# Performance work log

Hardware: AMD Instinct MI355X
Metric: run time of the kernel (lower is better)

The kernel has to match this reference:

```python
import jax, jax.numpy as jnp
import numpy as np

N = 50000      # nodes
E = 800000     # edges
H, C = 4, 32   # heads, per-head channels
NF = 513       # n_fft//2 + 1 frequency bins
NMEL = 128
NEG_SLOPE_ATT = 0.2   # GATConv leaky_relu slope
NEG_SLOPE_MLP = 0.01  # F.leaky_relu default


def setup_inputs() -> dict:
    key = jax.random.key(0)
    ks = jax.random.split(key, 12)
    s = 0.05
    return {
        "x": jax.random.normal(ks[0], (N, NF), jnp.float32),
        "edge_index": jax.random.randint(ks[1], (2, E), 0, N, dtype=jnp.int32),
        "fb": jax.random.normal(ks[2], (NF, NMEL), jnp.float32) * s,
        "Wg": jax.random.normal(ks[3], (NMEL, H * C), jnp.float32) * s,
        "bias_g": jnp.zeros((H * C,), jnp.float32),
        "att_src": jax.random.normal(ks[4], (H, C), jnp.float32) * s,
        "att_dst": jax.random.normal(ks[5], (H, C), jnp.float32) * s,
        "W1": jax.random.normal(ks[6], (H * C, 256), jnp.float32) * s,
        "b1": jnp.zeros((256,), jnp.float32),
        "W2": jax.random.normal(ks[7], (256, 128), jnp.float32) * s,
        "b2": jnp.zeros((128,), jnp.float32),
        "W3": jax.random.normal(ks[8], (128, 10), jnp.float32) * s,
        "b3": jnp.zeros((10,), jnp.float32),
    }


def gat_conv(h, src, dst, att_src, att_dst, bias_g):
    # h: [N, H, C]; per-edge attention, segment softmax over dst, scatter-add
    a_s = jnp.einsum('nhc,hc->nh', h, att_src)  # [N, H]
    a_d = jnp.einsum('nhc,hc->nh', h, att_dst)  # [N, H]
    e = jax.nn.leaky_relu(a_s[src] + a_d[dst], NEG_SLOPE_ATT)  # [E', H]
    m = jax.ops.segment_max(e, dst, num_segments=N)            # [N, H]
    ex = jnp.exp(e - m[dst])
    denom = jax.ops.segment_sum(ex, dst, num_segments=N)       # [N, H]
    alpha = ex / denom[dst]                                    # [E', H]
    msg = h[src] * alpha[:, :, None]                           # [E', H, C]
    out = jax.ops.segment_sum(msg, dst, num_segments=N)        # [N, H, C]
    return out.reshape(N, H * C) + bias_g


def reference(x, edge_index, fb, Wg, bias_g, att_src, att_dst, W1, b1, W2, b2, W3, b3):
    # learnable mel filterbank projection: [N, NF] -> [N, NMEL]
    x = x @ fb
    # GATConv linear transform, split into heads
    h = (x @ Wg).reshape(N, H, C)
    # add self loops (PyG GATConv default add_self_loops=True)
    loop = jnp.arange(N, dtype=edge_index.dtype)
    src = jnp.concatenate([edge_index[0], loop])
    dst = jnp.concatenate([edge_index[1], loop])
    x = jax.nn.elu(gat_conv(h, src, dst, att_src, att_dst, bias_g))
    # dropout is identity in eval mode
    x = jax.nn.leaky_relu(x @ W1 + b1, NEG_SLOPE_MLP)
    x = jax.nn.leaky_relu(x @ W2 + b2, NEG_SLOPE_MLP)
    x = jax.nn.leaky_relu(x @ W3 + b3, NEG_SLOPE_MLP)
    return jax.nn.softmax(x, axis=-1)
```

## Files before the change

### kernel.cpp

```cpp
#include <hip/hip_runtime.h>
#include <hip/hip_bf16.h>

#define NN 50000
#define EE 800000
#define NFR 513
#define NMEL 128
#define HC 128

typedef __bf16 bf16x8 __attribute__((ext_vector_type(8)));
typedef float floatx4 __attribute__((ext_vector_type(4)));

__device__ __forceinline__ unsigned short f2b(float f) {
    unsigned u = __float_as_uint(f);
    u = (u + 0x7FFFu + ((u >> 16) & 1u)) >> 16;
    return (unsigned short)u;
}
__device__ __forceinline__ float b2f(unsigned short s) {
    return __uint_as_float(((unsigned)s) << 16);
}
__device__ __forceinline__ float lexp(float a) {
    a = a > 0.f ? a : 0.2f * a;
    return __expf(a);
}

__device__ __forceinline__ float ldf(const float* p, long i) { return p[i]; }
__device__ __forceinline__ void stf(float* p, long i, float v) { p[i] = v; }
__device__ __forceinline__ void stf(__hip_bfloat16* p, long i, float v) {
    ((unsigned short*)p)[i] = f2b(v);
}

#define BM 64
#define BN 64
#define BK 16

template<int EPI, typename TA, typename TB, typename TC>
__global__ __launch_bounds__(256) void gemm_k(const TA* __restrict__ A, const TB* __restrict__ B,
                                              TC* __restrict__ C, int M, int Nn, int K,
                                              const float* __restrict__ bias)
{
    __shared__ float As[BK][BM + 4];
    __shared__ float Bs[BK][BN + 4];
    const int t = threadIdx.x;
    const int row0 = blockIdx.x * BM;
    const int col0 = blockIdx.y * BN;
    const int tc = t & 15, tr = t >> 4;
    float acc[4][4] = {};

    for (int kb = 0; kb < K; kb += BK) {
        #pragma unroll
        for (int i = 0; i < 4; ++i) {
            int idx = i * 256 + t;
            int r = idx >> 4, k = idx & 15;
            int gr = row0 + r, gk = kb + k;
            float v = 0.f;
            if (gr < M && gk < K) v = ldf(A, (long)gr * K + gk);
            As[k][r] = v;
        }
        #pragma unroll
        for (int i = 0; i < 4; ++i) {
            int idx = i * 256 + t;
            int c = idx & 63, k = idx >> 6;
            int gk = kb + k, gc = col0 + c;
            float v = 0.f;
            if (gk < K && gc < Nn) v = ldf(B, (long)gk * Nn + gc);
            Bs[k][c] = v;
        }
        __syncthreads();
        #pragma unroll
        for (int kk = 0; kk < BK; ++kk) {
            float4 av = *reinterpret_cast<const float4*>(&As[kk][tr << 2]);
            float4 bv = *reinterpret_cast<const float4*>(&Bs[kk][tc << 2]);
            float a[4] = {av.x, av.y, av.z, av.w};
            float b[4] = {bv.x, bv.y, bv.z, bv.w};
            #pragma unroll
            for (int i = 0; i < 4; ++i)
                #pragma unroll
                for (int j = 0; j < 4; ++j)
                    acc[i][j] += a[i] * b[j];
        }
        __syncthreads();
    }

    #pragma unroll
    for (int i = 0; i < 4; ++i) {
        int gr = row0 + (tr << 2) + i;
        if (gr >= M) continue;
        #pragma unroll
        for (int j = 0; j < 4; ++j) {
            int gc = col0 + (tc << 2) + j;
            if (gc >= Nn) continue;
            float v = acc[i][j];
            if (EPI == 2) {
                stf(C, (long)gc * 544 + gr, v);
            } else {
                if (EPI == 1) { v += bias[gc]; v = v > 0.f ? v : 0.01f * v; }
                stf(C, (long)gr * Nn + gc, v);
            }
        }
    }
}

__global__ void k_trans(const float* __restrict__ in, __hip_bfloat16* __restrict__ outp,
                        int K, int N, int KP)
{
    int id = blockIdx.x * 256 + threadIdx.x;
    if (id >= N * KP) return;
    int n = id / KP, k = id % KP;
    float v = (k < K) ? in[(long)k * N + n] : 0.f;
    ((unsigned short*)outp)[id] = f2b(v);
}

#define PS 40

__device__ __forceinline__ void stageA_t(const float* A, unsigned short* As, int t,
                                         int row0, int M, int K, int kb)
{
    #pragma unroll
    for (int g = 0; g < 2; ++g) {
        int q = g * 256 + t;
        int row = q >> 3, k4 = (q & 7) * 4;
        int gr = row0 + row, gk = kb + k4;
        ushort4 pk = make_ushort4(0, 0, 0, 0);
        if (gr < M) {
            const float* ap = A + (long)gr * K + gk;
            if (gk + 3 < K) {
                pk.x = f2b(ap[0]); pk.y = f2b(ap[1]); pk.z = f2b(ap[2]); pk.w = f2b(ap[3]);
            } else {
                if (gk + 0 < K) pk.x = f2b(ap[0]);
                if (gk + 1 < K) pk.y = f2b(ap[1]);
                if (gk + 2 < K) pk.z = f2b(ap[2]);
            }
        }
        *reinterpret_cast<ushort4*>(&As[row * PS + k4]) = pk;
    }
}

__device__ __forceinline__ void stageA_t(const __hip_bfloat16* A, unsigned short* As, int t,
                                         int row0, int M, int K, int kb)
{
    int c = t;
    int row = c >> 2, k8 = (c & 3) * 8;
    int gr = row0 + row;
    uint4 val = make_uint4(0, 0, 0, 0);
    if (gr < M) val = *reinterpret_cast<const uint4*>(A + (long)gr * K + kb + k8);
    *reinterpret_cast<uint4*>(&As[row * PS + k8]) = val;
}

template<int EPI, typename TA, typename TC>
__global__ __launch_bounds__(256) void mgemm(const TA* __restrict__ A,
                                             const __hip_bfloat16* __restrict__ Bt,
                                             TC* __restrict__ C,
                                             int M, int Nn, int K, int KB,
                                             const float* __restrict__ bias)
{
    __shared__ unsigned short As[64 * PS];
    __shared__ unsigned short Bs[128 * PS];
    const int t = threadIdx.x;
    const int row0 = blockIdx.x * 64;
    const int col0 = blockIdx.y * 128;
    const int wave = t >> 6, lane = t & 63;
    const int wm = (wave >> 1) * 32, wn = (wave & 1) * 64;
    const int lm = lane & 15, kq = lane >> 4;

    floatx4 acc[2][4];
    #pragma unroll
    for (int i = 0; i < 2; ++i)
        #pragma unroll
        for (int j = 0; j < 4; ++j)
            acc[i][j] = 0.f;

    for (int kb = 0; kb < KB; kb += 32) {
        stageA_t(A, As, t, row0, M, K, kb);
        #pragma unroll
        for (int g = 0; g < 2; ++g) {
            int c = g * 256 + t;
            int row = c >> 2, k8 = (c & 3) * 8;
            int gn = col0 + row;
            uint4 val = make_uint4(0, 0, 0, 0);
            if (gn < Nn) val = *reinterpret_cast<const uint4*>(Bt + (long)gn * KB + kb + k8);
            *reinterpret_cast<uint4*>(&Bs[row * PS + k8]) = val;
        }
        __syncthreads();

        bf16x8 af[2], bf[4];
        #pragma unroll
        for (int i = 0; i < 2; ++i)
            af[i] = *reinterpret_cast<const bf16x8*>(&As[(wm + i * 16 + lm) * PS + kq * 8]);
        #pragma unroll
        for (int j = 0; j < 4; ++j)
            bf[j] = *reinterpret_cast<const bf16x8*>(&Bs[(wn + j * 16 + lm) * PS + kq * 8]);
        #pragma unroll
        for (int i = 0; i < 2; ++i)
            #pragma unroll
            for (int j = 0; j < 4; ++j)
                acc[i][j] = __builtin_amdgcn_mfma_f32_16x16x32_bf16(af[i], bf[j], acc[i][j], 0, 0, 0);
        __syncthreads();
    }

    #pragma unroll
    for (int i = 0; i < 2; ++i) {
        #pragma unroll
        for (int r = 0; r < 4; ++r) {
            int gr = row0 + wm + i * 16 + kq * 4 + r;
            if (gr >= M) continue;
            #pragma unroll
            for (int j = 0; j < 4; ++j) {
                int gc = col0 + wn + j * 16 + lm;
                float v = acc[i][j][r];
                if (EPI == 1) { v += bias[gc]; v = v > 0.f ? v : 0.01f * v; }
                stf(C, (long)gr * Nn + gc, v);
            }
        }
    }
}

__global__ void k_att(const __hip_bfloat16* __restrict__ h, const float* __restrict__ att_src,
                      const float* __restrict__ att_dst,
                      float* __restrict__ a_s, float* __restrict__ a_d)
{
    int id = blockIdx.x * blockDim.x + threadIdx.x;
    if (id >= NN * 4) return;
    int n = id >> 2, hh = id & 3;
    const unsigned short* hr = (const unsigned short*)(h + (long)n * HC + hh * 32);
    float s1 = 0.f, s2 = 0.f;
    #pragma unroll
    for (int c = 0; c < 32; ++c) {
        float v = b2f(hr[c]);
        s1 += v * att_src[hh * 32 + c];
        s2 += v * att_dst[hh * 32 + c];
    }
    a_s[id] = s1;
    a_d[id] = s2;
}

__global__ void k_hist(const int* __restrict__ ei, int* __restrict__ hist)
{
    int e = blockIdx.x * 256 + threadIdx.x;
    if (e < EE) atomicAdd(&hist[ei[EE + e]], 1);
}

__global__ __launch_bounds__(512) void k_scan1(const int* __restrict__ hist, int* __restrict__ start,
                                               int* __restrict__ aux)
{
    __shared__ int sm[512];
    int t = threadIdx.x, i = blockIdx.x * 512 + t;
    int v = (i < NN) ? hist[i] : 0;
    sm[t] = v;
    __syncthreads();
    for (int off = 1; off < 512; off <<= 1) {
        int x = (t >= off) ? sm[t - off] : 0;
        __syncthreads();
        sm[t] += x;
        __syncthreads();
    }
    if (i < NN) start[i] = sm[t] - v;
    if (t == 511) aux[blockIdx.x] = sm[511];
}

__global__ void k_scan2(int* __restrict__ aux, int nb)
{
    if (blockIdx.x == 0 && threadIdx.x == 0) {
        int run = 0;
        for (int b = 0; b < nb; ++b) { int v = aux[b]; aux[b] = run; run += v; }
    }
}

__global__ __launch_bounds__(512) void k_scan3(int* __restrict__ start, int* __restrict__ cursor,
                                               const int* __restrict__ aux)
{
    int i = blockIdx.x * 512 + threadIdx.x;
    if (i < NN) {
        int v = start[i] + aux[blockIdx.x];
        start[i] = v;
        cursor[i] = v;
    }
    if (i == 0) start[NN] = EE;
}

__global__ void k_fill(const int* __restrict__ ei, int* __restrict__ cursor, int* __restrict__ sorted)
{
    int e = blockIdx.x * 256 + threadIdx.x;
    if (e >= EE) return;
    int s = ei[e], d = ei[EE + e];
    int pos = atomicAdd(&cursor[d], 1);
    sorted[pos] = s;
}

__global__ __launch_bounds__(256) void k_agg(const int* __restrict__ start, const int* __restrict__ sorted,
                                             const float* __restrict__ a_s, const float* __restrict__ a_d,
                                             const __hip_bfloat16* __restrict__ h,
                                             const float* __restrict__ bias_g,
                                             __hip_bfloat16* __restrict__ agg)
{
    int wave = threadIdx.x >> 6;
    int lane = threadIdx.x & 63;
    int d = blockIdx.x * 4 + wave;
    if (d >= NN) return;
    int hh = lane >> 4;
    float ad = a_d[d * 4 + hh];
    int e0 = start[d], e1 = start[d + 1];

    float ex = lexp(a_s[d * 4 + hh] + ad);
    unsigned hv = *reinterpret_cast<const unsigned*>(h + (long)d * HC + 2 * lane);
    float acc0 = ex * __uint_as_float(hv << 16);
    float acc1 = ex * __uint_as_float(hv & 0xffff0000u);
    float dsum = ex;

    int e = e0;
    for (; e + 4 <= e1; e += 4) {
        int s0 = sorted[e + 0], s1 = sorted[e + 1], s2 = sorted[e + 2], s3 = sorted[e + 3];
        float as0 = a_s[s0 * 4 + hh], as1 = a_s[s1 * 4 + hh];
        float as2 = a_s[s2 * 4 + hh], as3 = a_s[s3 * 4 + hh];
        unsigned h0 = *reinterpret_cast<const unsigned*>(h + (long)s0 * HC + 2 * lane);
        unsigned h1 = *reinterpret_cast<const unsigned*>(h + (long)s1 * HC + 2 * lane);
        unsigned h2 = *reinterpret_cast<const unsigned*>(h + (long)s2 * HC + 2 * lane);
        unsigned h3 = *reinterpret_cast<const unsigned*>(h + (long)s3 * HC + 2 * lane);
        float x0 = lexp(as0 + ad), x1 = lexp(as1 + ad), x2 = lexp(as2 + ad), x3 = lexp(as3 + ad);
        acc0 += x0 * __uint_as_float(h0 << 16);
        acc1 += x0 * __uint_as_float(h0 & 0xffff0000u);
        acc0 += x1 * __uint_as_float(h1 << 16);
        acc1 += x1 * __uint_as_float(h1 & 0xffff0000u);
        acc0 += x2 * __uint_as_float(h2 << 16);
        acc1 += x2 * __uint_as_float(h2 & 0xffff0000u);
        acc0 += x3 * __uint_as_float(h3 << 16);
        acc1 += x3 * __uint_as_float(h3 & 0xffff0000u);
        dsum += x0 + x1 + x2 + x3;
    }
    for (; e < e1; ++e) {
        int s = sorted[e];
        float xe = lexp(a_s[s * 4 + hh] + ad);
        unsigned hs = *reinterpret_cast<const unsigned*>(h + (long)s * HC + 2 * lane);
        acc0 += xe * __uint_as_float(hs << 16);
        acc1 += xe * __uint_as_float(hs & 0xffff0000u);
        dsum += xe;
    }

    float inv = 1.f / dsum;
    float2 bg = *reinterpret_cast<const float2*>(bias_g + 2 * lane);
    float v0 = acc0 * inv + bg.x;
    float v1 = acc1 * inv + bg.y;
    v0 = v0 > 0.f ? v0 : expm1f(v0);
    v1 = v1 > 0.f ? v1 : expm1f(v1);
    unsigned pk = (unsigned)f2b(v0) | ((unsigned)f2b(v1) << 16);
    *reinterpret_cast<unsigned*>((unsigned short*)agg + (long)d * HC + 2 * lane) = pk;
}

__global__ __launch_bounds__(256) void k_final(const __hip_bfloat16* __restrict__ x2, const float* __restrict__ W3,
                                               const float* __restrict__ b3, float* __restrict__ out)
{
    __shared__ float w3s[128 * 10];
    __shared__ float b3s[10];
    int t = threadIdx.x;
    for (int i = t; i < 128 * 10; i += 256) w3s[i] = W3[i];
    if (t < 10) b3s[t] = b3[t];
    __syncthreads();
    int n = blockIdx.x * 256 + t;
    if (n >= NN) return;

    float l[10];
    #pragma unroll
    for (int j = 0; j < 10; ++j) l[j] = b3s[j];
    const uint4* row = reinterpret_cast<const uint4*>(x2 + (long)n * 128);
    #pragma unroll 4
    for (int c8 = 0; c8 < 16; ++c8) {
        uint4 v = row[c8];
        const unsigned w[4] = {v.x, v.y, v.z, v.w};
        #pragma unroll
        for (int u = 0; u < 4; ++u) {
            float f0 = __uint_as_float(w[u] << 16);
            float f1 = __uint_as_float(w[u] & 0xffff0000u);
            const float* wr = &w3s[(c8 * 8 + u * 2) * 10];
            #pragma unroll
            for (int j = 0; j < 10; ++j) l[j] += f0 * wr[j] + f1 * wr[10 + j];
        }
    }
    float m = -1e30f;
    #pragma unroll
    for (int j = 0; j < 10; ++j) {
        float v = l[j];
        v = v > 0.f ? v : 0.01f * v;
        l[j] = v;
        m = fmaxf(m, v);
    }
    float sum = 0.f;
    #pragma unroll
    for (int j = 0; j < 10; ++j) { l[j] = __expf(l[j] - m); sum += l[j]; }
    float inv = 1.f / sum;
    #pragma unroll
    for (int j = 0; j < 10; ++j) out[(long)n * 10 + j] = l[j] * inv;
}

extern "C" void kernel_launch(void* const* d_in, const int* in_sizes, int n_in,
                              void* d_out, int out_size, void* d_ws, size_t ws_size,
                              hipStream_t stream)
{
    const float* x       = (const float*)d_in[0];
    const int*   ei      = (const int*)d_in[1];
    const float* fb      = (const float*)d_in[2];
    const float* Wg      = (const float*)d_in[3];
    const float* bias_g  = (const float*)d_in[4];
    const float* att_src = (const float*)d_in[5];
    const float* att_dst = (const float*)d_in[6];
    const float* W1      = (const float*)d_in[7];
    const float* b1      = (const float*)d_in[8];
    const float* W2      = (const float*)d_in[9];
    const float* b2      = (const float*)d_in[10];
    const float* W3      = (const float*)d_in[11];
    const float* b3      = (const float*)d_in[12];
    float* out = (float*)d_out;
    float* ws = (float*)d_ws;

    float* a_s = ws + 0;
    float* a_d = ws + 200000;
    __hip_bfloat16* fbWgT = (__hip_bfloat16*)(ws + 400000);
    __hip_bfloat16* W1T   = (__hip_bfloat16*)(ws + 434816);
    __hip_bfloat16* W2T   = (__hip_bfloat16*)(ws + 451200);
    int* hist   = (int*)(ws + 467584);
    int* startA = (int*)(ws + 517584);
    int* aux    = (int*)(ws + 567588);
    int* sorted = (int*)(ws + 567720);
    __hip_bfloat16* hbufB = (__hip_bfloat16*)(ws + 1367720);
    __hip_bfloat16* aggB  = (__hip_bfloat16*)(ws + 4567720);
    __hip_bfloat16* x1B   = (__hip_bfloat16*)(ws + 7767720);
    int* cursor = hist;
    __hip_bfloat16* x2B = hbufB;
    if (ws_size < (size_t)14167720 * sizeof(float)) return;

    hipMemsetAsync(ws + 400000, 0, (size_t)117584 * sizeof(float), stream);

    gemm_k<2, float, float, __hip_bfloat16><<<dim3(9, 2), 256, 0, stream>>>(fb, Wg, fbWgT, NFR, HC, NMEL, nullptr);
    k_trans<<<128, 256, 0, stream>>>(W1, W1T, 128, 256, 128);
    k_trans<<<128, 256, 0, stream>>>(W2, W2T, 256, 128, 256);

    mgemm<0, float, __hip_bfloat16><<<dim3(782, 1), 256, 0, stream>>>(x, fbWgT, hbufB, NN, HC, NFR, 544, nullptr);

    k_att<<<(NN * 4 + 255) / 256, 256, 0, stream>>>(hbufB, att_src, att_dst, a_s, a_d);

    k_hist<<<(EE + 255) / 256, 256, 0, stream>>>(ei, hist);
    k_scan1<<<98, 512, 0, stream>>>(hist, startA, aux);
    k_scan2<<<1, 64, 0, stream>>>(aux, 98);
    k_scan3<<<98, 512, 0, stream>>>(startA, cursor, aux);
    k_fill<<<(EE + 255) / 256, 256, 0, stream>>>(ei, cursor, sorted);

    k_agg<<<(NN + 3) / 4, 256, 0, stream>>>(startA, sorted, a_s, a_d, hbufB, bias_g, aggB);

    mgemm<1, __hip_bfloat16, __hip_bfloat16><<<dim3(782, 2), 256, 0, stream>>>(aggB, W1T, x1B, NN, 256, 128, 128, b1);

    mgemm<1, __hip_bfloat16, __hip_bfloat16><<<dim3(782, 1), 256, 0, stream>>>(x1B, W2T, x2B, NN, 128, 256, 256, b2);

    k_final<<<(NN + 255) / 256, 256, 0, stream>>>(x2B, W3, b3, out);
}
```

Before: 440.0 us.

## Double-buffer LDS tiles with register prefetch in the MFMA GEMM

The bf16 MFMA GEMM now stages its A and B tiles through a pair of LDS buffers. The next K-slice is loaded from global memory into registers while the current slice is being multiplied. This leaves one barrier per iteration instead of two and lets global-load latency overlap with MFMA work. The costs are doubled LDS per block and extra registers for the prefetched data, which could lower occupancy.

```diff
diff --git a/kernel.cpp b/kernel.cpp
--- a/kernel.cpp
+++ b/kernel.cpp
@@ -112,38 +112,85 @@
 
 #define PS 40
 
-__device__ __forceinline__ void stageA_t(const float* A, unsigned short* As, int t,
-                                         int row0, int M, int K, int kb)
+template<typename T> struct ARegs;
+template<> struct ARegs<float> { float v[8]; };
+template<> struct ARegs<__hip_bfloat16> { uint4 v; };
+
+__device__ __forceinline__ void loadA_r(const float* __restrict__ A, ARegs<float>& r, int t,
+                                        int row0, int M, int K, int kb)
 {
     #pragma unroll
     for (int g = 0; g < 2; ++g) {
         int q = g * 256 + t;
         int row = q >> 3, k4 = (q & 7) * 4;
         int gr = row0 + row, gk = kb + k4;
-        ushort4 pk = make_ushort4(0, 0, 0, 0);
+        float f0 = 0.f, f1 = 0.f, f2 = 0.f, f3 = 0.f;
         if (gr < M) {
             const float* ap = A + (long)gr * K + gk;
             if (gk + 3 < K) {
-                pk.x = f2b(ap[0]); pk.y = f2b(ap[1]); pk.z = f2b(ap[2]); pk.w = f2b(ap[3]);
+                f0 = ap[0]; f1 = ap[1]; f2 = ap[2]; f3 = ap[3];
             } else {
-                if (gk + 0 < K) pk.x = f2b(ap[0]);
-                if (gk + 1 < K) pk.y = f2b(ap[1]);
-                if (gk + 2 < K) pk.z = f2b(ap[2]);
+                if (gk + 0 < K) f0 = ap[0];
+                if (gk + 1 < K) f1 = ap[1];
+                if (gk + 2 < K) f2 = ap[2];
             }
         }
+        r.v[g * 4 + 0] = f0; r.v[g * 4 + 1] = f1;
+        r.v[g * 4 + 2] = f2; r.v[g * 4 + 3] = f3;
+    }
+}
+
+__device__ __forceinline__ void writeA_r(unsigned short* As, const ARegs<float>& r, int t)
+{
+    #pragma unroll
+    for (int g = 0; g < 2; ++g) {
+        int q = g * 256 + t;
+        int row = q >> 3, k4 = (q & 7) * 4;
+        ushort4 pk;
+        pk.x = f2b(r.v[g * 4 + 0]); pk.y = f2b(r.v[g * 4 + 1]);
+        pk.z = f2b(r.v[g * 4 + 2]); pk.w = f2b(r.v[g * 4 + 3]);
         *reinterpret_cast<ushort4*>(&As[row * PS + k4]) = pk;
     }
 }
 
-__device__ __forceinline__ void stageA_t(const __hip_bfloat16* A, unsigned short* As, int t,
-                                         int row0, int M, int K, int kb)
-{
-    int c = t;
-    int row = c >> 2, k8 = (c & 3) * 8;
+__device__ __forceinline__ void loadA_r(const __hip_bfloat16* __restrict__ A, ARegs<__hip_bfloat16>& r,
+                                        int t, int row0, int M, int K, int kb)
+{
+    int row = t >> 2, k8 = (t & 3) * 8;
     int gr = row0 + row;
     uint4 val = make_uint4(0, 0, 0, 0);
     if (gr < M) val = *reinterpret_cast<const uint4*>(A + (long)gr * K + kb + k8);
-    *reinterpret_cast<uint4*>(&As[row * PS + k8]) = val;
+    r.v = val;
+}
+
+__device__ __forceinline__ void writeA_r(unsigned short* As, const ARegs<__hip_bfloat16>& r, int t)
+{
+    int row = t >> 2, k8 = (t & 3) * 8;
+    *reinterpret_cast<uint4*>(&As[row * PS + k8]) = r.v;
+}
+
+__device__ __forceinline__ void loadB_r(const __hip_bfloat16* __restrict__ Bt, uint4* bR, int t,
+                                        int col0, int Nn, int KB, int kb)
+{
+    #pragma unroll
+    for (int g = 0; g < 2; ++g) {
+        int c = g * 256 + t;
+        int row = c >> 2, k8 = (c & 3) * 8;
+        int gn = col0 + row;
+        uint4 val = make_uint4(0, 0, 0, 0);
+        if (gn < Nn) val = *reinterpret_cast<const uint4*>(Bt + (long)gn * KB + kb + k8);
+        bR[g] = val;
+    }
+}
+
+__device__ __forceinline__ void writeB_r(unsigned short* Bs, const uint4* bR, int t)
+{
+    #pragma unroll
+    for (int g = 0; g < 2; ++g) {
+        int c = g * 256 + t;
+        int row = c >> 2, k8 = (c & 3) * 8;
+        *reinterpret_cast<uint4*>(&Bs[row * PS + k8]) = bR[g];
+    }
 }
 
 template<int EPI, typename TA, typename TC>
@@ -153,8 +200,8 @@
                                              int M, int Nn, int K, int KB,
                                              const float* __restrict__ bias)
 {
-    __shared__ unsigned short As[64 * PS];
-    __shared__ unsigned short Bs[128 * PS];
+    __shared__ unsigned short As[2][64 * PS];
+    __shared__ unsigned short Bs[2][128 * PS];
     const int t = threadIdx.x;
     const int row0 = blockIdx.x * 64;
     const int col0 = blockIdx.y * 128;
@@ -169,32 +216,37 @@
         for (int j = 0; j < 4; ++j)
             acc[i][j] = 0.f;
 
-    for (int kb = 0; kb < KB; kb += 32) {
-        stageA_t(A, As, t, row0, M, K, kb);
-        #pragma unroll
-        for (int g = 0; g < 2; ++g) {
-            int c = g * 256 + t;
-            int row = c >> 2, k8 = (c & 3) * 8;
-            int gn = col0 + row;
-            uint4 val = make_uint4(0, 0, 0, 0);
-            if (gn < Nn) val = *reinterpret_cast<const uint4*>(Bt + (long)gn * KB + kb + k8);
-            *reinterpret_cast<uint4*>(&Bs[row * PS + k8]) = val;
-        }
-        __syncthreads();
+    ARegs<TA> aR;
+    uint4 bR[2];
+    loadA_r(A, aR, t, row0, M, K, 0);
+    loadB_r(Bt, bR, t, col0, Nn, KB, 0);
+
+    const int nIter = KB >> 5;
+    int b = 0;
+    for (int it = 0; it < nIter; ++it) {
+        writeA_r(As[b], aR, t);
+        writeB_r(Bs[b], bR, t);
+        if (it + 1 < nIter) {
+            loadA_r(A, aR, t, row0, M, K, (it + 1) * 32);
+            loadB_r(Bt, bR, t, col0, Nn, KB, (it + 1) * 32);
+        }
+        asm volatile("s_waitcnt lgkmcnt(0)" ::: "memory");
+        __builtin_amdgcn_s_barrier();
+        __builtin_amdgcn_sched_barrier(0);
 
         bf16x8 af[2], bf[4];
         #pragma unroll
         for (int i = 0; i < 2; ++i)
-            af[i] = *reinterpret_cast<const bf16x8*>(&As[(wm + i * 16 + lm) * PS + kq * 8]);
+            af[i] = *reinterpret_cast<const bf16x8*>(&As[b][(wm + i * 16 + lm) * PS + kq * 8]);
         #pragma unroll
         for (int j = 0; j < 4; ++j)
-            bf[j] = *reinterpret_cast<const bf16x8*>(&Bs[(wn + j * 16 + lm) * PS + kq * 8]);
+            bf[j] = *reinterpret_cast<const bf16x8*>(&Bs[b][(wn + j * 16 + lm) * PS + kq * 8]);
         #pragma unroll
         for (int i = 0; i < 2; ++i)
             #pragma unroll
             for (int j = 0; j < 4; ++j)
                 acc[i][j] = __builtin_amdgcn_mfma_f32_16x16x32_bf16(af[i], bf[j], acc[i][j], 0, 0, 0);
-        __syncthreads();
+        b ^= 1;
     }
 
     #pragma unroll
```

Result: faster. 429.6 us (-2.4%).
